# Kernel tuning notes

Hardware: AMD Instinct MI355X
Metric: run time of the kernel (lower is better)

## Reference

```python
import jax, jax.numpy as jnp
import numpy as np

B, N1, N2 = 16, 4096, 1024
C1, C2 = 128, 256
IN_CH, OUT_CH = 4096, 256  # fc1 acts on N1 dim due to transpose; BN channels = C2 = OUT_CH
BN_EPS = 1e-5


def setup_inputs() -> dict:
    key = jax.random.key(0)
    ks = jax.random.split(key, 8)
    x1 = jax.random.normal(ks[0], (B, N1, C1), dtype=jnp.float32)
    x2 = jax.random.normal(ks[1], (B, N2, C2), dtype=jnp.float32)
    xyz1 = jax.random.normal(ks[2], (B, N1, 3), dtype=jnp.float32)
    xyz2 = jax.random.normal(ks[3], (B, N2, 3), dtype=jnp.float32)
    # Linear(in_channels=N1 -> out_channels) params, PyTorch default init scale
    bound = 1.0 / np.sqrt(IN_CH)
    W1 = jax.random.uniform(ks[4], (OUT_CH, IN_CH), jnp.float32, -bound, bound)
    b1 = jax.random.uniform(ks[5], (OUT_CH,), jnp.float32, -bound, bound)
    gamma = jnp.ones((OUT_CH,), jnp.float32)
    beta = jnp.zeros((OUT_CH,), jnp.float32)
    return {"x1": x1, "x2": x2, "xyz1": xyz1, "xyz2": xyz2,
            "W1": W1, "b1": b1, "gamma": gamma, "beta": beta}


def _square_distance(src, dst):
    # src: [B,N,3], dst: [B,M,3] -> [B,N,M]
    d = -2.0 * jnp.einsum('bnc,bmc->bnm', src, dst)
    d = d + jnp.sum(src * src, -1)[:, :, None]
    d = d + jnp.sum(dst * dst, -1)[:, None, :]
    return d


def reference(x1, x2, xyz1, xyz2, W1, b1, gamma, beta):
    dists = _square_distance(xyz1, xyz2)              # [B,N1,N2]
    neg3, idx = jax.lax.top_k(-dists, 3)              # 3 smallest distances
    d3 = -neg3                                        # [B,N1,3], ascending
    dist_recip = 1.0 / (d3 + 1e-8)
    weight = dist_recip / jnp.sum(dist_recip, axis=2, keepdims=True)
    gathered = jax.vmap(lambda pts, i: pts[i])(x2, idx)   # [B,N1,3,C2]
    interp = jnp.sum(gathered * weight[..., None], axis=2)  # [B,N1,C2]
    t = jnp.swapaxes(interp, 1, 2)                    # [B,C2,N1]
    y = jnp.einsum('bcn,on->bco', t, W1) + b1         # [B,C2,OUT_CH]
    # BatchNorm1d over channel dim 1 (size C2 == OUT_CH), training-mode batch stats
    mean = jnp.mean(y, axis=(0, 2), keepdims=True)
    var = jnp.mean((y - mean) ** 2, axis=(0, 2), keepdims=True)
    y = (y - mean) / jnp.sqrt(var + BN_EPS)
    y = gamma[None, :, None] * y + beta[None, :, None]
    y = jax.nn.relu(y)
    return jnp.swapaxes(y, 1, 2)                      # [B,OUT_CH,C2]
```

## Files before the change

### kernel.cpp

```cpp
#include <hip/hip_runtime.h>
#include <hip/hip_bf16.h>
#include <float.h>

#define B_    16
#define N1_   4096
#define N2_   1024
#define C2_   256
#define OUT_  256
#define K_    4096
#define SPLITK 8
#define KCH_  (K_ / SPLITK)
#define ZSLAB 1048576

typedef short short8 __attribute__((ext_vector_type(8)));
typedef float float4v __attribute__((ext_vector_type(4)));

static __device__ __forceinline__ unsigned short f32_to_bf16_bits(float v) {
    __hip_bfloat16 h = __float2bfloat16(v);
    return *(unsigned short*)&h;
}

static __device__ __forceinline__ void gload16(const void* g, void* l) {
    __builtin_amdgcn_global_load_lds(
        (const __attribute__((address_space(1))) unsigned int*)g,
        (__attribute__((address_space(3))) unsigned int*)l, 16, 0, 0);
}

#define TPAD 65
struct KnnSh {
    float4 pts[16][65];
    float  pf[64][49];
};
union ShUnion {
    KnnSh a;
    unsigned short tile[C2_][TPAD];
};

__global__ __launch_bounds__(256) void knn_interp_kernel(
    const float* __restrict__ xyz1,
    const float* __restrict__ xyz2,
    const float* __restrict__ x2,
    unsigned short* __restrict__ interp_t,
    const float* __restrict__ W1,
    unsigned short* __restrict__ W1b,
    float* __restrict__ accum)
{
    __shared__ ShUnion sh;
    __shared__ float rw[64][3];
    __shared__ int   ri[64][3];

    const int bid = blockIdx.x;
    const int t   = threadIdx.x;

    if (bid < 1024) {
        if (bid == 0) {
            accum[t] = 0.0f;
            accum[256 + t] = 0.0f;
        }
        const int i = (bid * 256 + t) * 4;
        float4 v = *(const float4*)(W1 + i);
        ushort4 o;
        o.x = f32_to_bf16_bits(v.x);
        o.y = f32_to_bf16_bits(v.y);
        o.z = f32_to_bf16_bits(v.z);
        o.w = f32_to_bf16_bits(v.w);
        *(ushort4*)(W1b + i) = o;
        return;
    }

    const int rem = bid - 1024;
    const int b   = ((rem >> 9) << 3) | (rem & 7);
    const int n0  = ((rem >> 3) & 63) * 64;
    const int w   = t >> 6;
    const int l   = t & 63;

    for (int r = 0; r < 4; ++r) {
        int j = r * 256 + t;
        const float* p = xyz2 + ((size_t)b * N2_ + j) * 3;
        float x = p[0], y = p[1], z = p[2];
        sh.a.pts[j >> 6][j & 63] = make_float4(x, y, z, 0.5f * ((x * x + y * y) + z * z));
    }
    __syncthreads();

    const int qg    = l & 15;
    const int slice = (w << 2) | (l >> 4);
    const int jbase = slice << 6;

    const float* qb = xyz1 + ((size_t)b * N1_ + n0 + qg * 4) * 3;
    float4 v0 = ((const float4*)qb)[0];
    float4 v1 = ((const float4*)qb)[1];
    float4 v2 = ((const float4*)qb)[2];
    float qx[4] = {v0.x, v0.w, v1.z, v2.y};
    float qy[4] = {v0.y, v1.x, v1.w, v2.z};
    float qz[4] = {v0.z, v1.y, v2.x, v2.w};

    float ns0[4], ns1[4], ns2[4], ss[4], f[4][3];
    #pragma unroll
    for (int i = 0; i < 4; ++i) {
        ns0[i] = -qx[i]; ns1[i] = -qy[i]; ns2[i] = -qz[i];
        ss[i]  = (qx[i] * qx[i] + qy[i] * qy[i]) + qz[i] * qz[i];
        f[i][0] = FLT_MAX; f[i][1] = FLT_MAX; f[i][2] = FLT_MAX;
    }

    #pragma unroll 2
    for (int jj = 0; jj < 64; ++jj) {
        float4 pq = sh.a.pts[slice][jj];
        int j = jbase + jj;
        #pragma unroll
        for (int i = 0; i < 4; ++i) {
            float acc = fmaf(ns0[i], pq.x, pq.w);
            acc = fmaf(ns1[i], pq.y, acc);
            acc = fmaf(ns2[i], pq.z, acc);
            float dk = fmaxf(fmaf(2.0f, acc, ss[i]), 0.0f);
            float fp = __int_as_float((__float_as_int(dk) & 0xFFFFFC00) | j);
            float nf0 = fminf(fp, f[i][0]);
            float nf1 = __builtin_amdgcn_fmed3f(fp, f[i][0], f[i][1]);
            float nf2 = fminf(f[i][2], fmaxf(fp, f[i][1]));
            f[i][0] = nf0; f[i][1] = nf1; f[i][2] = nf2;
        }
    }

    #pragma unroll
    for (int i = 0; i < 4; ++i)
    #pragma unroll
    for (int r = 0; r < 3; ++r)
        sh.a.pf[qg * 4 + i][slice * 3 + r] = f[i][r];
    __syncthreads();

    if (w == 0) {
        float g0 = FLT_MAX, g1 = FLT_MAX, g2 = FLT_MAX;
        #pragma unroll 4
        for (int s = 0; s < 16; ++s)
        #pragma unroll
        for (int r = 0; r < 3; ++r) {
            float fp = sh.a.pf[l][s * 3 + r];
            float n0v = fminf(fp, g0);
            float n1v = __builtin_amdgcn_fmed3f(fp, g0, g1);
            float n2v = fminf(g2, fmaxf(fp, g1));
            g0 = n0v; g1 = n1v; g2 = n2v;
        }
        int j0 = __float_as_int(g0) & 1023;
        int j1 = __float_as_int(g1) & 1023;
        int j2 = __float_as_int(g2) & 1023;
        const float4 p0 = sh.a.pts[j0 >> 6][j0 & 63];
        const float4 p1 = sh.a.pts[j1 >> 6][j1 & 63];
        const float4 p2 = sh.a.pts[j2 >> 6][j2 & 63];
        const float* q = xyz1 + ((size_t)b * N1_ + n0 + l) * 3;
        const float s0 = q[0], s1 = q[1], s2 = q[2];
        const float ssl = (s0 * s0 + s1 * s1) + s2 * s2;
        float dd0 = ssl + 2.0f * (p0.w - ((s0 * p0.x + s1 * p0.y) + s2 * p0.z));
        float dd1 = ssl + 2.0f * (p1.w - ((s0 * p1.x + s1 * p1.y) + s2 * p1.z));
        float dd2 = ssl + 2.0f * (p2.w - ((s0 * p2.x + s1 * p2.y) + s2 * p2.z));
        float r0 = 1.0f / (dd0 + 1e-8f);
        float r1 = 1.0f / (dd1 + 1e-8f);
        float r2 = 1.0f / (dd2 + 1e-8f);
        float sden = (r0 + r1) + r2;
        rw[l][0] = r0 / sden;  rw[l][1] = r1 / sden;  rw[l][2] = r2 / sden;
        ri[l][0] = j0;         ri[l][1] = j1;         ri[l][2] = j2;
    }
    __syncthreads();

    for (int p = 0; p < 16; ++p) {
        int nl = p * 4 + w;
        float w0 = rw[nl][0], w1 = rw[nl][1], w2 = rw[nl][2];
        int i0g = ri[nl][0], i1g = ri[nl][1], i2g = ri[nl][2];
        const float4 va = ((const float4*)(x2 + ((size_t)b * N2_ + i0g) * C2_))[l];
        const float4 vb = ((const float4*)(x2 + ((size_t)b * N2_ + i1g) * C2_))[l];
        const float4 vc = ((const float4*)(x2 + ((size_t)b * N2_ + i2g) * C2_))[l];
        float fa[4] = {va.x, va.y, va.z, va.w};
        float fb[4] = {vb.x, vb.y, vb.z, vb.w};
        float fc[4] = {vc.x, vc.y, vc.z, vc.w};
        #pragma unroll
        for (int i = 0; i < 4; ++i) {
            float v = w0 * fa[i];
            v = fmaf(w1, fb[i], v);
            v = fmaf(w2, fc[i], v);
            sh.tile[l * 4 + i][nl] = f32_to_bf16_bits(v);
        }
    }
    __syncthreads();

    for (int r = 0; r < 64; ++r) {
        int c = r * 4 + w;
        interp_t[((size_t)b * C2_ + c) * K_ + n0 + l] = sh.tile[c][l];
    }
}

__global__ __launch_bounds__(256) void gemm_kernel(
    const unsigned short* __restrict__ W1b,
    const unsigned short* __restrict__ interp_t,
    float* __restrict__ Zp)
{
    __shared__ unsigned short Alds[128 * 64];
    __shared__ unsigned short Blds[64 * 64];
    const int b  = blockIdx.y >> 3;
    const int kc = blockIdx.y & 7;
    const int o0 = blockIdx.z * 128;
    const int c0 = blockIdx.x * 64;
    const int t = threadIdx.x;
    const int w = t >> 6, l = t & 63;
    const int ob = (w >> 1) * 64, cb = (w & 1) * 32;
    const int m = l & 15, kq = l >> 4;

    const int rs  = l >> 3;
    const int ch  = l & 7;
    const int sch = ch ^ rs;

    const unsigned short* Abase = W1b + (size_t)o0 * K_ + kc * KCH_ + sch * 8;
    const unsigned short* Bbase = interp_t + ((size_t)b * C2_ + c0) * K_ + kc * KCH_ + sch * 8;

    float4v acc[4][2] = {};

    for (int kk = 0; kk < KCH_; kk += 64) {
        #pragma unroll
        for (int i = 0; i < 4; ++i) {
            int s = w + i * 4;
            gload16(Abase + (size_t)(s * 8 + rs) * K_ + kk, &Alds[s * 512 + l * 8]);
        }
        #pragma unroll
        for (int i = 0; i < 2; ++i) {
            int s = w + i * 4;
            gload16(Bbase + (size_t)(s * 8 + rs) * K_ + kk, &Blds[s * 512 + l * 8]);
        }
        __syncthreads();

        #pragma unroll
        for (int ks = 0; ks < 64; ks += 32) {
            const int swz = ((kq + (ks >> 3)) ^ (m & 7)) << 3;
            short8 bf0 = *(const short8*)&Blds[(cb + m) * 64 + swz];
            short8 bf1 = *(const short8*)&Blds[(cb + 16 + m) * 64 + swz];
            #pragma unroll
            for (int mi = 0; mi < 4; ++mi) {
                short8 af = *(const short8*)&Alds[(ob + mi * 16 + m) * 64 + swz];
                acc[mi][0] = __builtin_amdgcn_mfma_f32_16x16x32_bf16(af, bf0, acc[mi][0], 0, 0, 0);
                acc[mi][1] = __builtin_amdgcn_mfma_f32_16x16x32_bf16(af, bf1, acc[mi][1], 0, 0, 0);
            }
        }
        __syncthreads();
    }

    float* Zslab = Zp + (size_t)kc * ZSLAB;
    #pragma unroll
    for (int mi = 0; mi < 4; ++mi)
    #pragma unroll
    for (int ni = 0; ni < 2; ++ni)
    #pragma unroll
    for (int r = 0; r < 4; ++r) {
        int o = o0 + ob + mi * 16 + kq * 4 + r;
        int c = c0 + cb + ni * 16 + m;
        Zslab[((size_t)b * OUT_ + o) * C2_ + c] = acc[mi][ni][r];
    }
}

__global__ __launch_bounds__(256) void reduce_stats_kernel(
    float* __restrict__ Zp, const float* __restrict__ b1,
    float* __restrict__ accum)
{
    const int b  = blockIdx.x >> 4;
    const int oq = blockIdx.x & 15;
    const int c  = threadIdx.x;
    float s = 0.0f, s2 = 0.0f;
    for (int o16 = 0; o16 < 16; ++o16) {
        int o = oq * 16 + o16;
        size_t base = ((size_t)b * OUT_ + o) * C2_ + c;
        float v = b1[o];
        #pragma unroll
        for (int sl = 0; sl < SPLITK; ++sl)
            v += Zp[base + (size_t)sl * ZSLAB];
        Zp[base] = v;
        s += v; s2 += v * v;
    }
    atomicAdd(&accum[c], s);
    atomicAdd(&accum[C2_ + c], s2);
}

__global__ __launch_bounds__(256) void bn_kernel(
    const float* __restrict__ Z, const float* __restrict__ accum,
    const float* __restrict__ gamma, const float* __restrict__ beta,
    float* __restrict__ out)
{
    const int i = (blockIdx.x * 256 + threadIdx.x) * 4;
    float4 z = *(const float4*)(Z + i);
    float vals[4] = {z.x, z.y, z.z, z.w};
    const int cb = i & 255;
    float res[4];
    #pragma unroll
    for (int j = 0; j < 4; ++j) {
        int c = cb + j;
        float mean = accum[c] * (1.0f / 4096.0f);
        float var  = accum[C2_ + c] * (1.0f / 4096.0f) - mean * mean;
        float rstd = 1.0f / sqrtf(var + 1e-5f);
        float v = gamma[c] * ((vals[j] - mean) * rstd) + beta[c];
        res[j] = fmaxf(v, 0.0f);
    }
    *(float4*)(out + i) = make_float4(res[0], res[1], res[2], res[3]);
}

extern "C" void kernel_launch(void* const* d_in, const int* in_sizes, int n_in,
                              void* d_out, int out_size, void* d_ws, size_t ws_size,
                              hipStream_t stream) {
    const float* x2    = (const float*)d_in[1];
    const float* xyz1  = (const float*)d_in[2];
    const float* xyz2  = (const float*)d_in[3];
    const float* W1    = (const float*)d_in[4];
    const float* b1    = (const float*)d_in[5];
    const float* gamma = (const float*)d_in[6];
    const float* beta  = (const float*)d_in[7];

    char* ws = (char*)d_ws;
    unsigned short* interp_t = (unsigned short*)(ws);
    unsigned short* W1b      = (unsigned short*)(ws + 33554432);
    float*          Zp       = (float*)(ws + 35651584);
    float*          accum    = (float*)(ws + 69206016);

    knn_interp_kernel <<<2048, 256, 0, stream>>>(xyz1, xyz2, x2, interp_t,
                                                 W1, W1b, accum);
    gemm_kernel       <<<dim3(4, 128, 2), 256, 0, stream>>>(W1b, interp_t, Zp);
    reduce_stats_kernel<<<256, 256, 0, stream>>>(Zp, b1, accum);
    bn_kernel         <<<1024, 256, 0, stream>>>(Zp, accum, gamma, beta,
                                                 (float*)d_out);
}
```

Measured before the change: 152.8 us.

## Fuse split-K reduction and batchnorm into one kernel with grid barrier

Merges the split-K reduce/stats kernel and the batchnorm+ReLU kernel into a single launch. Each block keeps its 16 reduced values in registers, signals an atomic counter in workspace, and spins until all 256 blocks have contributed the channel sums. It then normalizes and writes the output directly. This removes one launch, the write-back of Z, and its re-read. The cost is a software grid barrier that depends on all 256 blocks being resident at the same time.

Result: slower. 177.4 us (+16.1%).

```diff
diff --git a/kernel.cpp b/kernel.cpp
--- a/kernel.cpp
+++ b/kernel.cpp
@@ -56,6 +56,7 @@
         if (bid == 0) {
             accum[t] = 0.0f;
             accum[256 + t] = 0.0f;
+            if (t == 0) accum[512] = 0.0f;
         }
         const int i = (bid * 256 + t) * 4;
         float4 v = *(const float4*)(W1 + i);
@@ -252,14 +253,18 @@
     }
 }
 
-__global__ __launch_bounds__(256) void reduce_stats_kernel(
-    float* __restrict__ Zp, const float* __restrict__ b1,
-    float* __restrict__ accum)
+__global__ __launch_bounds__(256) void reduce_bn_kernel(
+    const float* __restrict__ Zp, const float* __restrict__ b1,
+    float* __restrict__ accum,
+    const float* __restrict__ gamma, const float* __restrict__ beta,
+    float* __restrict__ out)
 {
     const int b  = blockIdx.x >> 4;
     const int oq = blockIdx.x & 15;
     const int c  = threadIdx.x;
+    float v16[16];
     float s = 0.0f, s2 = 0.0f;
+    #pragma unroll 4
     for (int o16 = 0; o16 < 16; ++o16) {
         int o = oq * 16 + o16;
         size_t base = ((size_t)b * OUT_ + o) * C2_ + c;
@@ -267,33 +272,35 @@
         #pragma unroll
         for (int sl = 0; sl < SPLITK; ++sl)
             v += Zp[base + (size_t)sl * ZSLAB];
-        Zp[base] = v;
+        v16[o16] = v;
         s += v; s2 += v * v;
     }
     atomicAdd(&accum[c], s);
     atomicAdd(&accum[C2_ + c], s2);
-}
-
-__global__ __launch_bounds__(256) void bn_kernel(
-    const float* __restrict__ Z, const float* __restrict__ accum,
-    const float* __restrict__ gamma, const float* __restrict__ beta,
-    float* __restrict__ out)
-{
-    const int i = (blockIdx.x * 256 + threadIdx.x) * 4;
-    float4 z = *(const float4*)(Z + i);
-    float vals[4] = {z.x, z.y, z.z, z.w};
-    const int cb = i & 255;
-    float res[4];
-    #pragma unroll
-    for (int j = 0; j < 4; ++j) {
-        int c = cb + j;
-        float mean = accum[c] * (1.0f / 4096.0f);
-        float var  = accum[C2_ + c] * (1.0f / 4096.0f) - mean * mean;
-        float rstd = 1.0f / sqrtf(var + 1e-5f);
-        float v = gamma[c] * ((vals[j] - mean) * rstd) + beta[c];
-        res[j] = fmaxf(v, 0.0f);
-    }
-    *(float4*)(out + i) = make_float4(res[0], res[1], res[2], res[3]);
+
+    __threadfence();
+    __syncthreads();
+    if (c == 0) {
+        unsigned int* cnt = (unsigned int*)(accum + 512);
+        atomicAdd(cnt, 1u);
+        while (__hip_atomic_load(cnt, __ATOMIC_ACQUIRE, __HIP_MEMORY_SCOPE_AGENT) < 256u) {
+            __builtin_amdgcn_s_sleep(8);
+        }
+    }
+    __syncthreads();
+
+    float sum  = __hip_atomic_load(&accum[c],        __ATOMIC_RELAXED, __HIP_MEMORY_SCOPE_AGENT);
+    float sum2 = __hip_atomic_load(&accum[C2_ + c],  __ATOMIC_RELAXED, __HIP_MEMORY_SCOPE_AGENT);
+    float mean = sum  * (1.0f / 4096.0f);
+    float var  = sum2 * (1.0f / 4096.0f) - mean * mean;
+    float rstd = 1.0f / sqrtf(var + 1e-5f);
+    float g = gamma[c], be = beta[c];
+    #pragma unroll 4
+    for (int o16 = 0; o16 < 16; ++o16) {
+        int o = oq * 16 + o16;
+        float v = g * ((v16[o16] - mean) * rstd) + be;
+        out[((size_t)b * OUT_ + o) * C2_ + c] = fmaxf(v, 0.0f);
+    }
 }
 
 extern "C" void kernel_launch(void* const* d_in, const int* in_sizes, int n_in,
@@ -316,7 +323,6 @@
     knn_interp_kernel <<<2048, 256, 0, stream>>>(xyz1, xyz2, x2, interp_t,
                                                  W1, W1b, accum);
     gemm_kernel       <<<dim3(4, 128, 2), 256, 0, stream>>>(W1b, interp_t, Zp);
-    reduce_stats_kernel<<<256, 256, 0, stream>>>(Zp, b1, accum);
-    bn_kernel         <<<1024, 256, 0, stream>>>(Zp, accum, gamma, beta,
-                                                 (float*)d_out);
-}
+    reduce_bn_kernel  <<<256, 256, 0, stream>>>(Zp, b1, accum, gamma, beta,
+                                                (float*)d_out);
+}
```
